# Kernel tuning notes

Hardware: AMD Instinct MI355X
Metric: run time of the kernel (lower is better)

Reference implementation:

```python
import jax, jax.numpy as jnp
from jax import lax
import numpy as np

B, T, H_IMG, W_IMG = 128, 64, 50, 60
Q_SIZE, R_SIZE, O_SIZE = 100, 100, 100
N_A = 4
H_SIZE = N_A * Q_SIZE  # 400
EMB = 750
OUT_CLASSES = 10
ALPHAS = jnp.array([0.0, 0.25, 0.5, 0.95], dtype=jnp.float32)


def setup_inputs() -> dict:
    key = jax.random.key(0)
    ks = jax.random.split(key, 14)
    s = 0.05
    return {
        "In": jax.random.normal(ks[0], (B, T, 1, H_IMG, W_IMG), dtype=jnp.float32),
        "conv1_w": jax.random.normal(ks[1], (16, 1, 3, 3), dtype=jnp.float32) * s,
        "conv1_b": jax.random.normal(ks[2], (16,), dtype=jnp.float32) * s,
        "conv2_w": jax.random.normal(ks[3], (1, 16, 3, 3), dtype=jnp.float32) * s,
        "conv2_b": jax.random.normal(ks[4], (1,), dtype=jnp.float32) * s,
        "R_w": jax.random.normal(ks[5], (H_SIZE, R_SIZE), dtype=jnp.float32) * s,
        "R_b": jax.random.normal(ks[6], (R_SIZE,), dtype=jnp.float32) * s,
        "Q_w": jax.random.normal(ks[7], (EMB + R_SIZE, Q_SIZE), dtype=jnp.float32) * s,
        "Q_b": jax.random.normal(ks[8], (Q_SIZE,), dtype=jnp.float32) * s,
        "O_w": jax.random.normal(ks[9], (H_SIZE, O_SIZE), dtype=jnp.float32) * s,
        "O_b": jax.random.normal(ks[10], (O_SIZE,), dtype=jnp.float32) * s,
        "Out_w": jax.random.normal(ks[11], (O_SIZE * T, OUT_CLASSES), dtype=jnp.float32) * s,
        "Out_b": jax.random.normal(ks[12], (OUT_CLASSES,), dtype=jnp.float32) * s,
    }


def _leaky(x):
    return jnp.where(x >= 0, x, 0.01 * x)  # LeakyReLU default slope


def reference(In, conv1_w, conv1_b, conv2_w, conv2_b, R_w, R_b, Q_w, Q_b,
              O_w, O_b, Out_w, Out_b):
    pad = ((1, 1), (1, 1))

    def embed(x):  # x: (B,1,50,60) -> (B,750)
        h = lax.conv_general_dilated(x, conv1_w, (1, 1), pad) + conv1_b[None, :, None, None]
        h = _leaky(h)
        h = lax.conv_general_dilated(h, conv2_w, (2, 2), pad) + conv2_b[None, :, None, None]
        h = _leaky(h)
        return h.reshape(h.shape[0], -1)

    def step(H_prev, x_t):  # H_prev: (B, 4, Q)
        bs = x_t.shape[0]
        Rt = jnp.tanh(H_prev.reshape(bs, H_SIZE) @ R_w + R_b)
        Qt = jnp.tanh(jnp.concatenate([embed(x_t), Rt], axis=1) @ Q_w + Q_b)
        Ha_t = ALPHAS[None, :, None] * H_prev + (1.0 - ALPHAS)[None, :, None] * Qt[:, None, :]
        Out_t = jnp.tanh(Ha_t.reshape(bs, H_SIZE) @ O_w + O_b)
        return Ha_t, Out_t

    bs = In.shape[0]
    xs = jnp.moveaxis(In, 0, 1)  # (T, B, 1, H, W)
    H0 = jnp.zeros((bs, N_A, Q_SIZE), dtype=In.dtype)
    _, Outs = lax.scan(step, H0, xs)  # (T, B, O_SIZE)
    Out = jnp.moveaxis(Outs, 0, 1).reshape(bs, -1)  # (B, T*O_SIZE)
    logits = Out @ Out_w + Out_b
    return jax.nn.softmax(logits, axis=1)
```

## Files before the change

kernel.cpp:

```cpp
#include <hip/hip_runtime.h>
#include <math.h>

#define B_ 128
#define T_ 64
#define PH2 54
#define PW2 64
#define EMB 750
#define MROW 819200

__device__ __forceinline__ float fast_tanh(float x) {
  float e = __expf(2.f * x);
  return 1.f - 2.f / (e + 1.f);
}

__device__ __forceinline__ float leaky(float x) {
  return fmaxf(x, 0.01f * x);
}

__global__ __launch_bounds__(256) void conv_embed_k(
    const float* __restrict__ In, const float* __restrict__ w1,
    const float* __restrict__ b1, const float* __restrict__ w2,
    const float* __restrict__ b2, float* __restrict__ E)
{
  __shared__ __align__(16) float sIn[PH2 * PW2];
  __shared__ __align__(16) float sAcc[768];

  const int tid = threadIdx.x;
  const int g = blockIdx.x;
  const int b = g >> 6;
  const int t = g & 63;
  const float* src = In + (size_t)g * 3000;

  float4 z4 = make_float4(0.f, 0.f, 0.f, 0.f);
  float4* sIn4 = (float4*)sIn;
  for (int i = tid; i < 864; i += 256) sIn4[i] = z4;
  float4* sAcc4 = (float4*)sAcc;
  for (int i = tid; i < 192; i += 256) sAcc4[i] = z4;
  __syncthreads();
  for (int i = tid; i < 3000; i += 256) {
    int y = i / 60, x = i - y * 60;
    sIn[(y + 2) * PW2 + (x + 2)] = src[i];
  }
  __syncthreads();

  for (int it = 0; it < 12; ++it) {
    const int id = tid + it * 256;
    if (id < 3000) {
      const int quad  = id / 750;
      const int rem   = id - quad * 750;
      const int rhalf = rem / 30;
      const int cc2   = rem - rhalf * 30;
      const int rp = quad >> 1, cp = quad & 1;
      const int r = 2 * rhalf + rp;
      const int c = 2 * cc2 + cp;

      float win[3][3];
      {
        const float* wb = &sIn[(r + 1) * PW2 + (c + 1)];
        #pragma unroll
        for (int ky = 0; ky < 3; ++ky) {
          #pragma unroll
          for (int kx = 0; kx < 3; ++kx) win[ky][kx] = wb[ky * PW2 + kx];
        }
      }

      auto c1v = [&](int ch) -> float {
        float a = b1[ch];
        #pragma unroll
        for (int ky = 0; ky < 3; ++ky) {
          a += w1[ch * 9 + ky * 3 + 0] * win[ky][0]
             + w1[ch * 9 + ky * 3 + 1] * win[ky][1]
             + w1[ch * 9 + ky * 3 + 2] * win[ky][2];
        }
        return leaky(a);
      };

      float s00 = 0.f, s01 = 0.f, s10 = 0.f, s11 = 0.f;
      if (quad == 0) {
        #pragma unroll
        for (int ch = 0; ch < 16; ++ch) { float a = c1v(ch); s00 += a * w2[ch * 9 + 4]; }
      } else if (quad == 1) {
        #pragma unroll
        for (int ch = 0; ch < 16; ++ch) {
          float a = c1v(ch);
          s00 += a * w2[ch * 9 + 5]; s01 += a * w2[ch * 9 + 3];
        }
      } else if (quad == 2) {
        #pragma unroll
        for (int ch = 0; ch < 16; ++ch) {
          float a = c1v(ch);
          s00 += a * w2[ch * 9 + 7]; s10 += a * w2[ch * 9 + 1];
        }
      } else {
        #pragma unroll
        for (int ch = 0; ch < 16; ++ch) {
          float a = c1v(ch);
          s00 += a * w2[ch * 9 + 8]; s01 += a * w2[ch * 9 + 6];
          s10 += a * w2[ch * 9 + 2]; s11 += a * w2[ch * 9 + 0];
        }
      }

      const int base = rhalf * 30 + cc2;
      atomicAdd(&sAcc[base], s00);
      if (cp && cc2 < 29)               atomicAdd(&sAcc[base + 1], s01);
      if (rp && rhalf < 24)             atomicAdd(&sAcc[base + 30], s10);
      if (rp && cp && rhalf < 24 && cc2 < 29) atomicAdd(&sAcc[base + 31], s11);
    }
  }
  __syncthreads();

  const float b2v = b2[0];
  float* erow = E + (size_t)(t * B_ + b) * EMB;
  for (int p = tid; p < 750; p += 256) erow[p] = leaky(sAcc[p] + b2v);
}

__global__ __launch_bounds__(256) void gemm_part_k(
    const float* __restrict__ A, const float* __restrict__ W,
    float* __restrict__ Part, int Ka, int tps)
{
  __shared__ __align__(16) float AsT[50 * 132];
  __shared__ __align__(16) float Ws[50 * 104];

  const int tid = threadIdx.x;
  const int m0 = blockIdx.x * 128;
  const int s  = blockIdx.y;
  const int ktotal = Ka / 50;
  const int kt0 = s * tps;
  const int nt  = min(tps, ktotal - kt0);
  float* part = Part + (size_t)s * MROW;

  const int rq = tid & 15;
  const int cq = tid >> 4;
  const bool active = (cq < 13);
  const int lr0 = rq * 8;
  const int c0 = cq * 8;

  float acc[8][8];
  #pragma unroll
  for (int r = 0; r < 8; ++r)
    #pragma unroll
    for (int c = 0; c < 8; ++c) acc[r][c] = 0.f;

  for (int kt = 0; kt < nt; ++kt) {
    const int k0 = (kt0 + kt) * 50;
    for (int i = tid; i < 6400; i += 256) {
      int r = i / 50, kk = i - r * 50;
      AsT[kk * 132 + r] = A[(size_t)(m0 + r) * Ka + k0 + kk];
    }
    for (int i = tid; i < 5000; i += 256) {
      int kk = i / 100, c = i - kk * 100;
      Ws[kk * 104 + c] = W[(size_t)(k0 + kk) * 100 + c];
    }
    __syncthreads();
    if (active) {
      for (int kk = 0; kk < 50; ++kk) {
        float4 a0 = *(const float4*)&AsT[kk * 132 + lr0];
        float4 a1 = *(const float4*)&AsT[kk * 132 + lr0 + 4];
        float4 w0 = *(const float4*)&Ws[kk * 104 + c0];
        float4 w1v = *(const float4*)&Ws[kk * 104 + c0 + 4];
        float av[8] = {a0.x, a0.y, a0.z, a0.w, a1.x, a1.y, a1.z, a1.w};
        float wv[8] = {w0.x, w0.y, w0.z, w0.w, w1v.x, w1v.y, w1v.z, w1v.w};
        #pragma unroll
        for (int r = 0; r < 8; ++r)
          #pragma unroll
          for (int c = 0; c < 8; ++c) acc[r][c] += av[r] * wv[c];
      }
    }
    __syncthreads();
  }

  if (active) {
    #pragma unroll
    for (int r = 0; r < 8; ++r) {
      float* pp = part + (size_t)(m0 + lr0 + r) * 100 + c0;
      *(float4*)pp = make_float4(acc[r][0], acc[r][1], acc[r][2], acc[r][3]);
      if (cq < 12)
        *(float4*)(pp + 4) = make_float4(acc[r][4], acc[r][5], acc[r][6], acc[r][7]);
    }
  }
}

__global__ __launch_bounds__(512) void scan_k(
    const float* __restrict__ EQp, const float* __restrict__ Qb,
    const float* __restrict__ Qw, const float* __restrict__ Rw,
    const float* __restrict__ Rb, float* __restrict__ Hf)
{
  __shared__ __align__(16) float sEQ[T_ * 100];
  __shared__ __align__(16) float sQ[100];
  __shared__ float sR[100];
  __shared__ float sGred[400];
  __shared__ float sP2[400];

  const int tid = threadIdx.x;
  const int b = blockIdx.x;
  const bool owner = (tid < 400);
  const int a = tid / 100;
  const int j = tid - a * 100;
  const float al = (a == 0) ? 0.f : (a == 1) ? 0.25f : (a == 2) ? 0.5f : 0.95f;

  {
    const float4* Qb4 = (const float4*)Qb;
    float4* sEQ4 = (float4*)sEQ;
    for (int i4 = tid; i4 < 1600; i4 += 512) {
      int tt = i4 / 25, j4 = i4 - tt * 25;
      size_t idx4 = (size_t)(tt * B_ + b) * 25 + j4;
      const float4* p0 = (const float4*)EQp;
      float4 v0 = p0[idx4];
      float4 v1 = p0[MROW / 4 + idx4];
      float4 v2 = p0[2 * (MROW / 4) + idx4];
      float4 v3 = p0[3 * (MROW / 4) + idx4];
      float4 qb = Qb4[j4];
      sEQ4[i4] = make_float4(v0.x + v1.x + v2.x + v3.x + qb.x,
                             v0.y + v1.y + v2.y + v3.y + qb.y,
                             v0.z + v1.z + v2.z + v3.z + qb.z,
                             v0.w + v1.w + v2.w + v3.w + qb.w);
    }
  }

  float rw[100];
  float qw[25];
  if (owner) {
    const float* rp = Rw + (size_t)a * 10000 + j;
    #pragma unroll
    for (int k = 0; k < 100; ++k) rw[k] = rp[(size_t)k * 100];
    const float* qp = Qw + (size_t)(750 + a * 25) * 100 + j;
    #pragma unroll
    for (int kk = 0; kk < 25; ++kk) qw[kk] = qp[(size_t)kk * 100];
    sGred[tid] = 0.f;
  }
  const float rb = (tid < 100) ? Rb[tid] : 0.f;
  float g = 0.f;
  float h1 = 0.f, h2 = 0.f, h3 = 0.f;
  __syncthreads();

  for (int t = 0; t < T_; ++t) {
    if (tid < 100) {
      float s = sGred[tid] + sGred[100 + tid] + sGred[200 + tid] + sGred[300 + tid] + rb;
      sR[tid] = fast_tanh(s);
    }
    __syncthreads();
    if (owner) {
      float p = 0.f;
      #pragma unroll
      for (int kk = 0; kk < 25; ++kk) p += sR[a * 25 + kk] * qw[kk];
      sP2[tid] = p;
    }
    __syncthreads();
    if (tid < 100) {
      float q = fast_tanh(sEQ[t * 100 + tid] +
                          sP2[tid] + sP2[100 + tid] + sP2[200 + tid] + sP2[300 + tid]);
      sQ[tid] = q;
      h1 = 0.25f * h1 + 0.75f * q;
      h2 = 0.50f * h2 + 0.50f * q;
      h3 = 0.95f * h3 + 0.05f * q;
      float* hp = Hf + (size_t)(t * B_ + b) * 400 + tid;
      hp[0] = q; hp[100] = h1; hp[200] = h2; hp[300] = h3;
    }
    __syncthreads();
    if (owner) {
      float d = 0.f;
      const float4* q4 = (const float4*)sQ;
      #pragma unroll
      for (int k4 = 0; k4 < 25; ++k4) {
        float4 qv = q4[k4];
        d += qv.x * rw[k4 * 4] + qv.y * rw[k4 * 4 + 1]
           + qv.z * rw[k4 * 4 + 2] + qv.w * rw[k4 * 4 + 3];
      }
      g = al * g + (1.f - al) * d;
      sGred[tid] = g;
    }
    __syncthreads();
  }
}

__global__ __launch_bounds__(256) void out_gemm_k(
    const float* __restrict__ Opart, const float* __restrict__ Ob,
    const float* __restrict__ OutW, float* __restrict__ Pl)
{
  __shared__ float sW[1000];
  __shared__ float sOb[100];
  const int tid = threadIdx.x;
  const int kb = blockIdx.x;
  for (int i = tid; i < 1000; i += 256) sW[i] = OutW[kb * 1000 + i];
  if (tid < 100) sOb[tid] = Ob[tid];
  __syncthreads();

  const int bb = tid >> 1;
  const int half = tid & 1;
  const size_t row = (size_t)kb * B_ + bb;
  float acc[10];
  #pragma unroll
  for (int c = 0; c < 10; ++c) acc[c] = 0.f;

  for (int kk = 0; kk < 50; ++kk) {
    const int off = half * 50 + kk;
    const size_t idx = row * 100 + off;
    float p = Opart[idx] + Opart[MROW + idx] + Opart[2 * MROW + idx] + Opart[3 * MROW + idx];
    float o = fast_tanh(p + sOb[off]);
    const float* w = &sW[off * 10];
    #pragma unroll
    for (int c = 0; c < 10; ++c) acc[c] += o * w[c];
  }
  #pragma unroll
  for (int c = 0; c < 10; ++c) acc[c] += __shfl_xor(acc[c], 1, 2);
  if (half == 0) {
    float* pp = &Pl[(size_t)kb * 1280 + bb * 10];
    #pragma unroll
    for (int c = 0; c < 10; ++c) pp[c] = acc[c];
  }
}

__global__ __launch_bounds__(64) void softmax_k(
    const float* __restrict__ Pl, const float* __restrict__ OutB,
    float* __restrict__ out)
{
  const int b = blockIdx.x;
  const int lane = threadIdx.x;
  float acc[10];
  const float* pp = &Pl[(size_t)lane * 1280 + b * 10];
  #pragma unroll
  for (int c = 0; c < 10; ++c) acc[c] = pp[c];
  #pragma unroll
  for (int sdl = 32; sdl >= 1; sdl >>= 1) {
    #pragma unroll
    for (int c = 0; c < 10; ++c) acc[c] += __shfl_down(acc[c], sdl, 64);
  }
  if (lane == 0) {
    float lg[10];
    #pragma unroll
    for (int c = 0; c < 10; ++c) lg[c] = acc[c] + OutB[c];
    float mx = lg[0];
    #pragma unroll
    for (int c = 1; c < 10; ++c) mx = fmaxf(mx, lg[c]);
    float e[10], ssum = 0.f;
    #pragma unroll
    for (int c = 0; c < 10; ++c) { e[c] = expf(lg[c] - mx); ssum += e[c]; }
    float inv = 1.f / ssum;
    #pragma unroll
    for (int c = 0; c < 10; ++c) out[b * 10 + c] = e[c] * inv;
  }
}

extern "C" void kernel_launch(void* const* d_in, const int* in_sizes, int n_in,
                              void* d_out, int out_size, void* d_ws, size_t ws_size,
                              hipStream_t stream)
{
  const float* In   = (const float*)d_in[0];
  const float* w1   = (const float*)d_in[1];
  const float* b1   = (const float*)d_in[2];
  const float* w2   = (const float*)d_in[3];
  const float* b2   = (const float*)d_in[4];
  const float* Rw   = (const float*)d_in[5];
  const float* Rb   = (const float*)d_in[6];
  const float* Qw   = (const float*)d_in[7];
  const float* Qb   = (const float*)d_in[8];
  const float* Ow   = (const float*)d_in[9];
  const float* Ob   = (const float*)d_in[10];
  const float* OutW = (const float*)d_in[11];
  const float* OutB = (const float*)d_in[12];
  float* out = (float*)d_out;

  float* ws  = (float*)d_ws;
  float* E   = ws;
  float* EQp = E + 6144000;
  float* Hf  = EQp + 4 * MROW;
  float* Op  = EQp;
  float* Pl  = E;

  hipLaunchKernelGGL(conv_embed_k, dim3(B_ * T_), dim3(256), 0, stream,
                     In, w1, b1, w2, b2, E);
  hipLaunchKernelGGL(gemm_part_k, dim3(64, 4), dim3(256), 0, stream,
                     E, Qw, EQp, 750, 4);
  hipLaunchKernelGGL(scan_k, dim3(B_), dim3(512), 0, stream,
                     EQp, Qb, Qw, Rw, Rb, Hf);
  hipLaunchKernelGGL(gemm_part_k, dim3(64, 4), dim3(256), 0, stream,
                     Hf, Ow, Op, 400, 2);
  hipLaunchKernelGGL(out_gemm_k, dim3(64), dim3(256), 0, stream,
                     Op, Ob, OutW, Pl);
  hipLaunchKernelGGL(softmax_k, dim3(B_), dim3(64), 0, stream,
                     Pl, OutB, out);
}
```

Before: 653.8 us.

## Register-block conv embed, vectorize GEMM tile loads, stage tanh outputs in LDS

The conv embedding kernel now has each thread compute a strip of 12 conv1 columns over all 16 channels from one register window loaded once from LDS. Each thread accumulates 7 outputs of the stride-2 conv2, which cuts redundant window loads and the number of shared atomics. The GEMM partial kernel loads A with float2 and W with float4 instead of scalar loads. The output GEMM first reduces the split-K partials and applies tanh into shared memory with coalesced loads, replacing strided per-thread global reads. The new kernels use more registers and more LDS (about 55KB in out_gemm), which may lower occupancy.

```diff
diff --git a/kernel.cpp b/kernel.cpp
--- a/kernel.cpp
+++ b/kernel.cpp
@@ -3,7 +3,7 @@
 
 #define B_ 128
 #define T_ 64
-#define PH2 54
+#define PH_ 52
 #define PW2 64
 #define EMB 750
 #define MROW 819200
@@ -22,7 +22,7 @@
     const float* __restrict__ b1, const float* __restrict__ w2,
     const float* __restrict__ b2, float* __restrict__ E)
 {
-  __shared__ __align__(16) float sIn[PH2 * PW2];
+  __shared__ __align__(16) float sIn[PH_ * PW2];
   __shared__ __align__(16) float sAcc[768];
 
   const int tid = threadIdx.x;
@@ -33,78 +33,94 @@
 
   float4 z4 = make_float4(0.f, 0.f, 0.f, 0.f);
   float4* sIn4 = (float4*)sIn;
-  for (int i = tid; i < 864; i += 256) sIn4[i] = z4;
+  for (int i = tid; i < 832; i += 256) sIn4[i] = z4;
   float4* sAcc4 = (float4*)sAcc;
   for (int i = tid; i < 192; i += 256) sAcc4[i] = z4;
   __syncthreads();
   for (int i = tid; i < 3000; i += 256) {
     int y = i / 60, x = i - y * 60;
-    sIn[(y + 2) * PW2 + (x + 2)] = src[i];
-  }
-  __syncthreads();
-
-  for (int it = 0; it < 12; ++it) {
-    const int id = tid + it * 256;
-    if (id < 3000) {
-      const int quad  = id / 750;
-      const int rem   = id - quad * 750;
-      const int rhalf = rem / 30;
-      const int cc2   = rem - rhalf * 30;
-      const int rp = quad >> 1, cp = quad & 1;
-      const int r = 2 * rhalf + rp;
-      const int c = 2 * cc2 + cp;
-
-      float win[3][3];
-      {
-        const float* wb = &sIn[(r + 1) * PW2 + (c + 1)];
+    sIn[(y + 1) * PW2 + (x + 1)] = src[i];
+  }
+  __syncthreads();
+
+  const int rp = tid >> 7;
+  const int sub = tid & 127;
+  const bool act = (sub < 125);
+  const int rI = sub / 5;
+  const int run = sub - rI * 5;
+  const int r = 2 * rI + rp;
+  const int x0 = 12 * run;
+  const int cb = 6 * run;
+
+  float acc[2][7];
+  #pragma unroll
+  for (int q = 0; q < 7; ++q) { acc[0][q] = 0.f; acc[1][q] = 0.f; }
+
+  if (act) {
+    float win[3][14];
+    const float* wb = &sIn[r * PW2 + x0];
+    #pragma unroll
+    for (int wr = 0; wr < 3; ++wr) {
+      const float2* rp2 = (const float2*)(wb + wr * PW2);
+      #pragma unroll
+      for (int q = 0; q < 7; ++q) {
+        float2 v = rp2[q];
+        win[wr][2 * q] = v.x; win[wr][2 * q + 1] = v.y;
+      }
+    }
+
+    #pragma unroll 1
+    for (int cg = 0; cg < 4; ++cg) {
+      #pragma unroll
+      for (int cc = 0; cc < 4; ++cc) {
+        const int ch = cg * 4 + cc;
+        float wv[9], w2v[9];
         #pragma unroll
-        for (int ky = 0; ky < 3; ++ky) {
+        for (int q = 0; q < 9; ++q) { wv[q] = w1[ch * 9 + q]; w2v[q] = w2[ch * 9 + q]; }
+        const float bias = b1[ch];
+
+        #pragma unroll
+        for (int u = 0; u < 12; ++u) {
+          float a = bias;
           #pragma unroll
-          for (int kx = 0; kx < 3; ++kx) win[ky][kx] = wb[ky * PW2 + kx];
+          for (int ky = 0; ky < 3; ++ky) {
+            a += wv[ky * 3 + 0] * win[ky][u + 0]
+               + wv[ky * 3 + 1] * win[ky][u + 1]
+               + wv[ky * 3 + 2] * win[ky][u + 2];
+          }
+          a = leaky(a);
+          if (rp == 0) {
+            if ((u & 1) == 0) {
+              acc[0][u / 2] += a * w2v[4];
+            } else {
+              acc[0][(u - 1) / 2] += a * w2v[5];
+              acc[0][(u + 1) / 2] += a * w2v[3];
+            }
+          } else {
+            if ((u & 1) == 0) {
+              acc[0][u / 2] += a * w2v[7];
+              acc[1][u / 2] += a * w2v[1];
+            } else {
+              acc[0][(u - 1) / 2] += a * w2v[8];
+              acc[0][(u + 1) / 2] += a * w2v[6];
+              acc[1][(u - 1) / 2] += a * w2v[2];
+              acc[1][(u + 1) / 2] += a * w2v[0];
+            }
+          }
         }
       }
-
-      auto c1v = [&](int ch) -> float {
-        float a = b1[ch];
-        #pragma unroll
-        for (int ky = 0; ky < 3; ++ky) {
-          a += w1[ch * 9 + ky * 3 + 0] * win[ky][0]
-             + w1[ch * 9 + ky * 3 + 1] * win[ky][1]
-             + w1[ch * 9 + ky * 3 + 2] * win[ky][2];
-        }
-        return leaky(a);
-      };
-
-      float s00 = 0.f, s01 = 0.f, s10 = 0.f, s11 = 0.f;
-      if (quad == 0) {
-        #pragma unroll
-        for (int ch = 0; ch < 16; ++ch) { float a = c1v(ch); s00 += a * w2[ch * 9 + 4]; }
-      } else if (quad == 1) {
-        #pragma unroll
-        for (int ch = 0; ch < 16; ++ch) {
-          float a = c1v(ch);
-          s00 += a * w2[ch * 9 + 5]; s01 += a * w2[ch * 9 + 3];
-        }
-      } else if (quad == 2) {
-        #pragma unroll
-        for (int ch = 0; ch < 16; ++ch) {
-          float a = c1v(ch);
-          s00 += a * w2[ch * 9 + 7]; s10 += a * w2[ch * 9 + 1];
-        }
-      } else {
-        #pragma unroll
-        for (int ch = 0; ch < 16; ++ch) {
-          float a = c1v(ch);
-          s00 += a * w2[ch * 9 + 8]; s01 += a * w2[ch * 9 + 6];
-          s10 += a * w2[ch * 9 + 2]; s11 += a * w2[ch * 9 + 0];
-        }
+    }
+
+    const int rowbase = rI * 30 + cb;
+    #pragma unroll
+    for (int jl = 0; jl < 7; ++jl) {
+      if (cb + jl < 30) atomicAdd(&sAcc[rowbase + jl], acc[0][jl]);
+    }
+    if (rp == 1 && rI < 24) {
+      #pragma unroll
+      for (int jl = 0; jl < 7; ++jl) {
+        if (cb + jl < 30) atomicAdd(&sAcc[rowbase + 30 + jl], acc[1][jl]);
       }
-
-      const int base = rhalf * 30 + cc2;
-      atomicAdd(&sAcc[base], s00);
-      if (cp && cc2 < 29)               atomicAdd(&sAcc[base + 1], s01);
-      if (rp && rhalf < 24)             atomicAdd(&sAcc[base + 30], s10);
-      if (rp && cp && rhalf < 24 && cc2 < 29) atomicAdd(&sAcc[base + 31], s11);
     }
   }
   __syncthreads();
@@ -143,13 +159,16 @@
 
   for (int kt = 0; kt < nt; ++kt) {
     const int k0 = (kt0 + kt) * 50;
-    for (int i = tid; i < 6400; i += 256) {
-      int r = i / 50, kk = i - r * 50;
-      AsT[kk * 132 + r] = A[(size_t)(m0 + r) * Ka + k0 + kk];
-    }
-    for (int i = tid; i < 5000; i += 256) {
-      int kk = i / 100, c = i - kk * 100;
-      Ws[kk * 104 + c] = W[(size_t)(k0 + kk) * 100 + c];
+    for (int i = tid; i < 3200; i += 256) {
+      int rr = i / 25, kk2 = (i - rr * 25) * 2;
+      float2 v = *(const float2*)&A[(size_t)(m0 + rr) * Ka + k0 + kk2];
+      AsT[kk2 * 132 + rr] = v.x;
+      AsT[(kk2 + 1) * 132 + rr] = v.y;
+    }
+    for (int i = tid; i < 1250; i += 256) {
+      int kk = i / 25, c4 = (i - kk * 25) * 4;
+      float4 v = *(const float4*)&W[(size_t)(k0 + kk) * 100 + c4];
+      *(float4*)&Ws[kk * 104 + c4] = v;
     }
     __syncthreads();
     if (active) {
@@ -277,26 +296,30 @@
     const float* __restrict__ Opart, const float* __restrict__ Ob,
     const float* __restrict__ OutW, float* __restrict__ Pl)
 {
-  __shared__ float sW[1000];
-  __shared__ float sOb[100];
+  __shared__ float sW[1104];
+  __shared__ float sO[12800];
   const int tid = threadIdx.x;
   const int kb = blockIdx.x;
   for (int i = tid; i < 1000; i += 256) sW[i] = OutW[kb * 1000 + i];
-  if (tid < 100) sOb[tid] = Ob[tid];
+  if (tid < 100) sW[1000 + tid] = Ob[tid];
+  __syncthreads();
+
+  for (int i = tid; i < 12800; i += 256) {
+    const size_t idx = (size_t)kb * 12800 + i;
+    float p = Opart[idx] + Opart[MROW + idx] + Opart[2 * MROW + idx] + Opart[3 * MROW + idx];
+    sO[i] = fast_tanh(p + sW[1000 + (i - (i / 100) * 100)]);
+  }
   __syncthreads();
 
   const int bb = tid >> 1;
   const int half = tid & 1;
-  const size_t row = (size_t)kb * B_ + bb;
   float acc[10];
   #pragma unroll
   for (int c = 0; c < 10; ++c) acc[c] = 0.f;
 
   for (int kk = 0; kk < 50; ++kk) {
     const int off = half * 50 + kk;
-    const size_t idx = row * 100 + off;
-    float p = Opart[idx] + Opart[MROW + idx] + Opart[2 * MROW + idx] + Opart[3 * MROW + idx];
-    float o = fast_tanh(p + sOb[off]);
+    float o = sO[bb * 100 + off];
     const float* w = &sW[off * 10];
     #pragma unroll
     for (int c = 0; c < 10; ++c) acc[c] += o * w[c];
```

Measured after the change: 563.3 us. 1.16x faster.
